# Performance work log

Hardware: AMD Instinct MI355X
Metric: run time of the kernel (lower is better)

## Reference

```python
import jax, jax.numpy as jnp
import numpy as np

HUGE = jnp.float32(1e31)   # ops.HUGE_INT
EPS = 1e-20
B, AN = 1024, 256
D = 256            # emb_dim
HD = 512           # history_dim
AD = 2 * D         # action_dim
NE, NR = 100000, 400


def setup_inputs() -> dict:
    key = jax.random.key(0)
    ks = jax.random.split(key, 12)
    e = jax.random.randint(ks[0], (B,), 0, NE)
    q = jax.random.randint(ks[1], (B,), 0, NR)
    hstate = jax.random.normal(ks[2], (B, HD), dtype=jnp.float32)
    r_space = jax.random.randint(ks[3], (B, AN), 0, NR)
    e_space = jax.random.randint(ks[4], (B, AN), 0, NE)
    # binary action mask; guarantee at least one valid action per row
    action_mask = (jax.random.uniform(ks[5], (B, AN)) > 0.2).astype(jnp.float32)
    action_mask = action_mask.at[:, 0].set(1.0)
    entity_emb = jax.random.normal(ks[6], (NE, D), dtype=jnp.float32) * 0.02
    relation_emb = jax.random.normal(ks[7], (NR, D), dtype=jnp.float32) * 0.02
    W1 = jax.random.normal(ks[8], (2 * D + HD, AD), dtype=jnp.float32) * (1.0 / np.sqrt(2 * D + HD))
    b1 = jnp.zeros((AD,), dtype=jnp.float32)
    W2 = jax.random.normal(ks[9], (AD, AD), dtype=jnp.float32) * (1.0 / np.sqrt(AD))
    b2 = jnp.zeros((AD,), dtype=jnp.float32)
    return {"e": e, "q": q, "hstate": hstate, "r_space": r_space,
            "e_space": e_space, "action_mask": action_mask,
            "entity_emb": entity_emb, "relation_emb": relation_emb,
            "W1": W1, "b1": b1, "W2": W2, "b2": b2}


def reference(e, q, hstate, r_space, e_space, action_mask,
              entity_emb, relation_emb, W1, b1, W2, b2):
    Q = relation_emb[q]                       # [B, D]
    E = entity_emb[e]                         # [B, D]
    X = jnp.concatenate([E, hstate, Q], axis=-1)          # [B, 2D+HD]
    X = jax.nn.relu(X @ W1 + b1)                          # [B, AD]
    X2 = X @ W2 + b2                                      # [B, AD]
    # action embeddings: [rel_emb[r]; ent_emb[e]] per padded action slot
    A = jnp.concatenate([relation_emb[r_space], entity_emb[e_space]], axis=-1)  # [B, AN, AD]
    scores = jnp.einsum('bad,bd->ba', A, X2) - (1.0 - action_mask) * HUGE      # [B, AN]
    action_dist = jax.nn.softmax(scores, axis=-1)
    entropy = -jnp.sum(action_dist * jnp.log(jnp.clip(action_dist, EPS)), axis=-1)  # [B]
    return action_dist, entropy
```

## Files before the change

kernel.cpp:

```cpp
#include <hip/hip_runtime.h>
#include <math.h>

#define NB   1024
#define NACT 256
#define DIM  256
#define HDIM 512
#define ADIM 512
#define KTOT 1024
#define KSPL 8

#define BM 64
#define BN 64
#define BK 32
#define LDA 68
#define LDB 68

__global__ __launch_bounds__(256) void gemm1_splitk(
    const int* __restrict__ e, const int* __restrict__ q,
    const float* __restrict__ hstate,
    const float* __restrict__ ent, const float* __restrict__ rel,
    const float* __restrict__ W1, float* __restrict__ Hpart)
{
    __shared__ float As[BK][LDA];
    __shared__ float Bs[BK][LDB];
    const int tid  = threadIdx.x;
    const int col0 = blockIdx.x * BN;
    const int row0 = blockIdx.y * BM;
    const int kc   = blockIdx.z;
    const int kbase = kc * (KTOT / KSPL);
    const int tx4  = (tid & 15) * 4;
    const int ty4  = (tid >> 4) * 4;
    float acc[4][4] = {};

    for (int k0 = 0; k0 < KTOT / KSPL; k0 += BK) {
        const int kglob = kbase + k0;
        #pragma unroll
        for (int s = 0; s < 2; ++s) {
            const int idx = tid * 2 + s;
            const int m   = idx >> 3;
            const int kf  = (idx & 7) * 4;
            const int b   = row0 + m;
            const int kk2 = kglob + kf;
            const float* src;
            if (kbase < DIM)             src = ent + (size_t)e[b] * DIM + kk2;
            else if (kbase < DIM + HDIM) src = hstate + (size_t)b * HDIM + (kk2 - DIM);
            else                         src = rel + (size_t)q[b] * DIM + (kk2 - DIM - HDIM);
            const float4 v = *(const float4*)src;
            As[kf + 0][m] = v.x;
            As[kf + 1][m] = v.y;
            As[kf + 2][m] = v.z;
            As[kf + 3][m] = v.w;
        }
        #pragma unroll
        for (int s = 0; s < 2; ++s) {
            const int idx = tid * 2 + s;
            const int k   = idx >> 4;
            const int n4  = (idx & 15) * 4;
            const float4 v = *(const float4*)(W1 + (size_t)(kglob + k) * ADIM + col0 + n4);
            *(float4*)(&Bs[k][n4]) = v;
        }
        __syncthreads();
        #pragma unroll
        for (int kk = 0; kk < BK; ++kk) {
            const float4 a4 = *(const float4*)(&As[kk][ty4]);
            const float4 b4 = *(const float4*)(&Bs[kk][tx4]);
            const float a[4] = {a4.x, a4.y, a4.z, a4.w};
            const float bb[4] = {b4.x, b4.y, b4.z, b4.w};
            #pragma unroll
            for (int i = 0; i < 4; ++i)
                #pragma unroll
                for (int j = 0; j < 4; ++j)
                    acc[i][j] += a[i] * bb[j];
        }
        __syncthreads();
    }
    float* dst = Hpart + (size_t)kc * NB * ADIM;
    #pragma unroll
    for (int i = 0; i < 4; ++i) {
        float4 o = {acc[i][0], acc[i][1], acc[i][2], acc[i][3]};
        *(float4*)(dst + (size_t)(row0 + ty4 + i) * ADIM + col0 + tx4) = o;
    }
}

__global__ __launch_bounds__(256) void gemm2_splitk(
    const float* __restrict__ Hpart, const float* __restrict__ b1,
    const float* __restrict__ W2, float* __restrict__ X2part)
{
    __shared__ float As[BK][LDA];
    __shared__ float Bs[BK][LDB];
    const int tid  = threadIdx.x;
    const int col0 = blockIdx.x * BN;
    const int row0 = blockIdx.y * BM;
    const int kc   = blockIdx.z;
    const int tx4  = (tid & 15) * 4;
    const int ty4  = (tid >> 4) * 4;
    float acc[4][4] = {};

    for (int k0 = 0; k0 < ADIM / KSPL; k0 += BK) {
        const int kglob = kc * (ADIM / KSPL) + k0;
        #pragma unroll
        for (int s = 0; s < 2; ++s) {
            const int idx = tid * 2 + s;
            const int m   = idx >> 3;
            const int kf  = (idx & 7) * 4;
            const int b   = row0 + m;
            const size_t off = (size_t)b * ADIM + kglob + kf;
            float4 v = *(const float4*)(b1 + kglob + kf);
            #pragma unroll
            for (int z = 0; z < KSPL; ++z) {
                const float4 p = *(const float4*)(Hpart + (size_t)z * NB * ADIM + off);
                v.x += p.x; v.y += p.y; v.z += p.z; v.w += p.w;
            }
            v.x = fmaxf(v.x, 0.0f);
            v.y = fmaxf(v.y, 0.0f);
            v.z = fmaxf(v.z, 0.0f);
            v.w = fmaxf(v.w, 0.0f);
            As[kf + 0][m] = v.x;
            As[kf + 1][m] = v.y;
            As[kf + 2][m] = v.z;
            As[kf + 3][m] = v.w;
        }
        #pragma unroll
        for (int s = 0; s < 2; ++s) {
            const int idx = tid * 2 + s;
            const int k   = idx >> 4;
            const int n4  = (idx & 15) * 4;
            const float4 v = *(const float4*)(W2 + (size_t)(kglob + k) * ADIM + col0 + n4);
            *(float4*)(&Bs[k][n4]) = v;
        }
        __syncthreads();
        #pragma unroll
        for (int kk = 0; kk < BK; ++kk) {
            const float4 a4 = *(const float4*)(&As[kk][ty4]);
            const float4 b4 = *(const float4*)(&Bs[kk][tx4]);
            const float a[4] = {a4.x, a4.y, a4.z, a4.w};
            const float bb[4] = {b4.x, b4.y, b4.z, b4.w};
            #pragma unroll
            for (int i = 0; i < 4; ++i)
                #pragma unroll
                for (int j = 0; j < 4; ++j)
                    acc[i][j] += a[i] * bb[j];
        }
        __syncthreads();
    }
    float* dst = X2part + (size_t)kc * NB * ADIM;
    #pragma unroll
    for (int i = 0; i < 4; ++i) {
        float4 o = {acc[i][0], acc[i][1], acc[i][2], acc[i][3]};
        *(float4*)(dst + (size_t)(row0 + ty4 + i) * ADIM + col0 + tx4) = o;
    }
}

__global__ __launch_bounds__(512) void scores_kernel(
    const int* __restrict__ r_space, const int* __restrict__ e_space,
    const float* __restrict__ amask,
    const float* __restrict__ ent, const float* __restrict__ rel,
    const float* __restrict__ X2part, const float* __restrict__ b2,
    float* __restrict__ dist_out, float* __restrict__ ent_out)
{
    const int b    = blockIdx.x;
    const int tid  = threadIdx.x;
    const int wave = tid >> 6;
    const int lane = tid & 63;

    __shared__ float xs[ADIM];
    __shared__ float sc[NACT];
    __shared__ float red1[8], red2[8], red3[8];

    if (tid < ADIM / 4) {
        float4 v = ((const float4*)b2)[tid];
        #pragma unroll
        for (int z = 0; z < KSPL; ++z) {
            const float4 p = ((const float4*)(X2part + (size_t)z * NB * ADIM + (size_t)b * ADIM))[tid];
            v.x += p.x; v.y += p.y; v.z += p.z; v.w += p.w;
        }
        ((float4*)xs)[tid] = v;
    }
    __syncthreads();

    const float4 xr = ((const float4*)xs)[lane];
    const float4 xe = ((const float4*)(xs + DIM))[lane];

    const int abase = wave * 32;
    for (int a0 = abase; a0 < abase + 32; a0 += 8) {
        float p[8];
        #pragma unroll
        for (int i = 0; i < 8; ++i) {
            const int r  = r_space[(size_t)b * NACT + a0 + i];
            const int ei = e_space[(size_t)b * NACT + a0 + i];
            const float4 rv = ((const float4*)(rel + (size_t)r  * DIM))[lane];
            const float4 ev = ((const float4*)(ent + (size_t)ei * DIM))[lane];
            p[i] = rv.x * xr.x + rv.y * xr.y + rv.z * xr.z + rv.w * xr.w
                 + ev.x * xe.x + ev.y * xe.y + ev.z * xe.z + ev.w * xe.w;
        }
        #pragma unroll
        for (int off = 32; off; off >>= 1) {
            #pragma unroll
            for (int i = 0; i < 8; ++i) p[i] += __shfl_xor(p[i], off);
        }
        if (lane < 8) sc[a0 + lane] = p[lane];
    }
    __syncthreads();

    float s = -3.0e38f;
    if (tid < NACT) {
        const float m = amask[(size_t)b * NACT + tid];
        s = sc[tid] - (1.0f - m) * 1e31f;
    }

    float mx = s;
    #pragma unroll
    for (int off = 32; off; off >>= 1) mx = fmaxf(mx, __shfl_xor(mx, off));
    if (lane == 0) red1[wave] = mx;
    __syncthreads();
    mx = red1[0];
    #pragma unroll
    for (int w = 1; w < 8; ++w) mx = fmaxf(mx, red1[w]);

    const float ex = (tid < NACT) ? expf(s - mx) : 0.0f;
    float sum = ex;
    #pragma unroll
    for (int off = 32; off; off >>= 1) sum += __shfl_xor(sum, off);
    if (lane == 0) red2[wave] = sum;
    __syncthreads();
    sum = ((red2[0] + red2[1]) + (red2[2] + red2[3]))
        + ((red2[4] + red2[5]) + (red2[6] + red2[7]));

    const float d = ex / sum;
    if (tid < NACT) dist_out[(size_t)b * NACT + tid] = d;

    float t = (tid < NACT) ? d * logf(fmaxf(d, 1e-20f)) : 0.0f;
    #pragma unroll
    for (int off = 32; off; off >>= 1) t += __shfl_xor(t, off);
    if (lane == 0) red3[wave] = t;
    __syncthreads();
    if (tid == 0)
        ent_out[b] = -(((red3[0] + red3[1]) + (red3[2] + red3[3]))
                     + ((red3[4] + red3[5]) + (red3[6] + red3[7])));
}

extern "C" void kernel_launch(void* const* d_in, const int* in_sizes, int n_in,
                              void* d_out, int out_size, void* d_ws, size_t ws_size,
                              hipStream_t stream) {
    const int*   e       = (const int*)d_in[0];
    const int*   q       = (const int*)d_in[1];
    const float* hstate  = (const float*)d_in[2];
    const int*   r_space = (const int*)d_in[3];
    const int*   e_space = (const int*)d_in[4];
    const float* amask   = (const float*)d_in[5];
    const float* ent     = (const float*)d_in[6];
    const float* rel     = (const float*)d_in[7];
    const float* W1      = (const float*)d_in[8];
    const float* b1      = (const float*)d_in[9];
    const float* W2      = (const float*)d_in[10];
    const float* b2      = (const float*)d_in[11];

    float* Hpart  = (float*)d_ws;
    float* X2part = Hpart + (size_t)KSPL * NB * ADIM;
    float* dist   = (float*)d_out;
    float* entr   = dist + (size_t)NB * NACT;

    gemm1_splitk<<<dim3(ADIM / BN, NB / BM, KSPL), 256, 0, stream>>>(e, q, hstate, ent, rel, W1, Hpart);
    gemm2_splitk<<<dim3(ADIM / BN, NB / BM, KSPL), 256, 0, stream>>>(Hpart, b1, W2, X2part);
    scores_kernel<<<NB, 512, 0, stream>>>(r_space, e_space, amask, ent, rel, X2part, b2, dist, entr);
}
```

Measured before the change: 241.1 us.

## Convert embedding tables to bf16 each call, pipeline GEMM loads, split out reduce

The first GEMM kernel now also converts the full entity and relation tables to bf16 on every call. The scores kernel then gathers half-width rows for its per-action dot products, which cuts gather bandwidth at the cost of a full-table read and write each call and some precision loss. Both GEMMs get register prefetch of the next K tile to overlap global loads with compute. The split-K reduction, bias and ReLU move into a separate kernel instead of being recomputed in every gemm2 block. Index arrays are staged in shared memory.

```diff
diff --git a/kernel.cpp b/kernel.cpp
--- a/kernel.cpp
+++ b/kernel.cpp
@@ -8,6 +8,8 @@
 #define ADIM 512
 #define KTOT 1024
 #define KSPL 8
+#define NE   100000
+#define NR   400
 
 #define BM 64
 #define BN 64
@@ -15,56 +17,179 @@
 #define LDA 68
 #define LDB 68
 
+__device__ __forceinline__ unsigned short f2bf(float f) {
+    unsigned int u = __float_as_uint(f);
+    u += 0x7FFF + ((u >> 16) & 1);
+    return (unsigned short)(u >> 16);
+}
+__device__ __forceinline__ float bf2f(unsigned short u) {
+    return __uint_as_float(((unsigned int)u) << 16);
+}
+
 __global__ __launch_bounds__(256) void gemm1_splitk(
     const int* __restrict__ e, const int* __restrict__ q,
     const float* __restrict__ hstate,
     const float* __restrict__ ent, const float* __restrict__ rel,
-    const float* __restrict__ W1, float* __restrict__ Hpart)
+    const float* __restrict__ W1, float* __restrict__ Hpart,
+    ushort* __restrict__ entbf, ushort* __restrict__ relbf)
+{
+    const int tid = threadIdx.x;
+    {
+        const int flat = blockIdx.x + blockIdx.y * gridDim.x
+                       + blockIdx.z * gridDim.x * gridDim.y;
+        const float4* src = (const float4*)ent;
+        ushort4* dst = (ushort4*)entbf;
+        const int start = flat * 6250;
+        #pragma unroll 4
+        for (int j = start + tid; j < start + 6250; j += 256) {
+            const float4 v = src[j];
+            ushort4 o;
+            o.x = f2bf(v.x); o.y = f2bf(v.y); o.z = f2bf(v.z); o.w = f2bf(v.w);
+            dst[j] = o;
+        }
+        if (tid < 25) {
+            const int j = flat * 25 + tid;
+            const float4 v = ((const float4*)rel)[j];
+            ushort4 o;
+            o.x = f2bf(v.x); o.y = f2bf(v.y); o.z = f2bf(v.z); o.w = f2bf(v.w);
+            ((ushort4*)relbf)[j] = o;
+        }
+    }
+
+    __shared__ float As[BK][LDA];
+    __shared__ float Bs[BK][LDB];
+    const int col0 = blockIdx.x * BN;
+    const int row0 = blockIdx.y * BM;
+    const int kbase = blockIdx.z * (KTOT / KSPL);
+    const int tx4 = (tid & 15) * 4;
+    const int ty4 = (tid >> 4) * 4;
+
+    const int am  = tid & 63;
+    const int kf0 = (tid >> 6) * 4;
+    const float* abase;
+    if (kbase < DIM)             abase = ent + (size_t)e[row0 + am] * DIM + kbase;
+    else if (kbase < DIM + HDIM) abase = hstate + (size_t)(row0 + am) * HDIM + (kbase - DIM);
+    else                         abase = rel + (size_t)q[row0 + am] * DIM + (kbase - DIM - HDIM);
+
+    const int kb0 = tid >> 4;
+    const float* bbase = W1 + col0 + tx4;
+
+    float4 pa0 = *(const float4*)(abase + kf0);
+    float4 pa1 = *(const float4*)(abase + kf0 + 16);
+    float4 pb0 = *(const float4*)(bbase + (size_t)(kbase + kb0) * ADIM);
+    float4 pb1 = *(const float4*)(bbase + (size_t)(kbase + kb0 + 16) * ADIM);
+
+    float acc[4][4] = {};
+    #pragma unroll
+    for (int it = 0; it < (KTOT / KSPL) / BK; ++it) {
+        As[kf0 + 0][am] = pa0.x;
+        As[kf0 + 1][am] = pa0.y;
+        As[kf0 + 2][am] = pa0.z;
+        As[kf0 + 3][am] = pa0.w;
+        As[kf0 + 16][am] = pa1.x;
+        As[kf0 + 17][am] = pa1.y;
+        As[kf0 + 18][am] = pa1.z;
+        As[kf0 + 19][am] = pa1.w;
+        *(float4*)(&Bs[kb0][tx4])      = pb0;
+        *(float4*)(&Bs[kb0 + 16][tx4]) = pb1;
+        __syncthreads();
+        if (it < (KTOT / KSPL) / BK - 1) {
+            const int ko = (it + 1) * BK;
+            pa0 = *(const float4*)(abase + ko + kf0);
+            pa1 = *(const float4*)(abase + ko + kf0 + 16);
+            pb0 = *(const float4*)(bbase + (size_t)(kbase + ko + kb0) * ADIM);
+            pb1 = *(const float4*)(bbase + (size_t)(kbase + ko + kb0 + 16) * ADIM);
+        }
+        #pragma unroll
+        for (int kk = 0; kk < BK; ++kk) {
+            const float4 a4 = *(const float4*)(&As[kk][ty4]);
+            const float4 b4 = *(const float4*)(&Bs[kk][tx4]);
+            const float a[4]  = {a4.x, a4.y, a4.z, a4.w};
+            const float bb[4] = {b4.x, b4.y, b4.z, b4.w};
+            #pragma unroll
+            for (int i = 0; i < 4; ++i)
+                #pragma unroll
+                for (int j = 0; j < 4; ++j)
+                    acc[i][j] += a[i] * bb[j];
+        }
+        __syncthreads();
+    }
+    float* dst = Hpart + (size_t)blockIdx.z * NB * ADIM;
+    #pragma unroll
+    for (int i = 0; i < 4; ++i) {
+        float4 o = {acc[i][0], acc[i][1], acc[i][2], acc[i][3]};
+        *(float4*)(dst + (size_t)(row0 + ty4 + i) * ADIM + col0 + tx4) = o;
+    }
+}
+
+__global__ __launch_bounds__(256) void reduce_relu(
+    const float* __restrict__ Hpart, const float* __restrict__ b1,
+    float* __restrict__ Hred)
+{
+    const int i = blockIdx.x * 256 + threadIdx.x;
+    float4 v = ((const float4*)b1)[i & 127];
+    #pragma unroll
+    for (int z = 0; z < KSPL; ++z) {
+        const float4 p = ((const float4*)Hpart)[(size_t)z * (NB * ADIM / 4) + i];
+        v.x += p.x; v.y += p.y; v.z += p.z; v.w += p.w;
+    }
+    v.x = fmaxf(v.x, 0.0f);
+    v.y = fmaxf(v.y, 0.0f);
+    v.z = fmaxf(v.z, 0.0f);
+    v.w = fmaxf(v.w, 0.0f);
+    ((float4*)Hred)[i] = v;
+}
+
+__global__ __launch_bounds__(256) void gemm2_splitk(
+    const float* __restrict__ Hred, const float* __restrict__ W2,
+    float* __restrict__ X2part)
 {
     __shared__ float As[BK][LDA];
     __shared__ float Bs[BK][LDB];
     const int tid  = threadIdx.x;
     const int col0 = blockIdx.x * BN;
     const int row0 = blockIdx.y * BM;
-    const int kc   = blockIdx.z;
-    const int kbase = kc * (KTOT / KSPL);
-    const int tx4  = (tid & 15) * 4;
-    const int ty4  = (tid >> 4) * 4;
+    const int kbase = blockIdx.z * (ADIM / KSPL);
+    const int tx4 = (tid & 15) * 4;
+    const int ty4 = (tid >> 4) * 4;
+
+    const int am  = tid & 63;
+    const int kf0 = (tid >> 6) * 4;
+    const float* abase = Hred + (size_t)(row0 + am) * ADIM + kbase;
+    const int kb0 = tid >> 4;
+    const float* bbase = W2 + col0 + tx4;
+
+    float4 pa0 = *(const float4*)(abase + kf0);
+    float4 pa1 = *(const float4*)(abase + kf0 + 16);
+    float4 pb0 = *(const float4*)(bbase + (size_t)(kbase + kb0) * ADIM);
+    float4 pb1 = *(const float4*)(bbase + (size_t)(kbase + kb0 + 16) * ADIM);
+
     float acc[4][4] = {};
-
-    for (int k0 = 0; k0 < KTOT / KSPL; k0 += BK) {
-        const int kglob = kbase + k0;
-        #pragma unroll
-        for (int s = 0; s < 2; ++s) {
-            const int idx = tid * 2 + s;
-            const int m   = idx >> 3;
-            const int kf  = (idx & 7) * 4;
-            const int b   = row0 + m;
-            const int kk2 = kglob + kf;
-            const float* src;
-            if (kbase < DIM)             src = ent + (size_t)e[b] * DIM + kk2;
-            else if (kbase < DIM + HDIM) src = hstate + (size_t)b * HDIM + (kk2 - DIM);
-            else                         src = rel + (size_t)q[b] * DIM + (kk2 - DIM - HDIM);
-            const float4 v = *(const float4*)src;
-            As[kf + 0][m] = v.x;
-            As[kf + 1][m] = v.y;
-            As[kf + 2][m] = v.z;
-            As[kf + 3][m] = v.w;
-        }
-        #pragma unroll
-        for (int s = 0; s < 2; ++s) {
-            const int idx = tid * 2 + s;
-            const int k   = idx >> 4;
-            const int n4  = (idx & 15) * 4;
-            const float4 v = *(const float4*)(W1 + (size_t)(kglob + k) * ADIM + col0 + n4);
-            *(float4*)(&Bs[k][n4]) = v;
-        }
+    #pragma unroll
+    for (int it = 0; it < (ADIM / KSPL) / BK; ++it) {
+        As[kf0 + 0][am] = pa0.x;
+        As[kf0 + 1][am] = pa0.y;
+        As[kf0 + 2][am] = pa0.z;
+        As[kf0 + 3][am] = pa0.w;
+        As[kf0 + 16][am] = pa1.x;
+        As[kf0 + 17][am] = pa1.y;
+        As[kf0 + 18][am] = pa1.z;
+        As[kf0 + 19][am] = pa1.w;
+        *(float4*)(&Bs[kb0][tx4])      = pb0;
+        *(float4*)(&Bs[kb0 + 16][tx4]) = pb1;
         __syncthreads();
+        if (it < (ADIM / KSPL) / BK - 1) {
+            const int ko = (it + 1) * BK;
+            pa0 = *(const float4*)(abase + ko + kf0);
+            pa1 = *(const float4*)(abase + ko + kf0 + 16);
+            pb0 = *(const float4*)(bbase + (size_t)(kbase + ko + kb0) * ADIM);
+            pb1 = *(const float4*)(bbase + (size_t)(kbase + ko + kb0 + 16) * ADIM);
+        }
         #pragma unroll
         for (int kk = 0; kk < BK; ++kk) {
             const float4 a4 = *(const float4*)(&As[kk][ty4]);
             const float4 b4 = *(const float4*)(&Bs[kk][tx4]);
-            const float a[4] = {a4.x, a4.y, a4.z, a4.w};
+            const float a[4]  = {a4.x, a4.y, a4.z, a4.w};
             const float bb[4] = {b4.x, b4.y, b4.z, b4.w};
             #pragma unroll
             for (int i = 0; i < 4; ++i)
@@ -74,7 +199,7 @@
         }
         __syncthreads();
     }
-    float* dst = Hpart + (size_t)kc * NB * ADIM;
+    float* dst = X2part + (size_t)blockIdx.z * NB * ADIM;
     #pragma unroll
     for (int i = 0; i < 4; ++i) {
         float4 o = {acc[i][0], acc[i][1], acc[i][2], acc[i][3]};
@@ -82,79 +207,10 @@
     }
 }
 
-__global__ __launch_bounds__(256) void gemm2_splitk(
-    const float* __restrict__ Hpart, const float* __restrict__ b1,
-    const float* __restrict__ W2, float* __restrict__ X2part)
-{
-    __shared__ float As[BK][LDA];
-    __shared__ float Bs[BK][LDB];
-    const int tid  = threadIdx.x;
-    const int col0 = blockIdx.x * BN;
-    const int row0 = blockIdx.y * BM;
-    const int kc   = blockIdx.z;
-    const int tx4  = (tid & 15) * 4;
-    const int ty4  = (tid >> 4) * 4;
-    float acc[4][4] = {};
-
-    for (int k0 = 0; k0 < ADIM / KSPL; k0 += BK) {
-        const int kglob = kc * (ADIM / KSPL) + k0;
-        #pragma unroll
-        for (int s = 0; s < 2; ++s) {
-            const int idx = tid * 2 + s;
-            const int m   = idx >> 3;
-            const int kf  = (idx & 7) * 4;
-            const int b   = row0 + m;
-            const size_t off = (size_t)b * ADIM + kglob + kf;
-            float4 v = *(const float4*)(b1 + kglob + kf);
-            #pragma unroll
-            for (int z = 0; z < KSPL; ++z) {
-                const float4 p = *(const float4*)(Hpart + (size_t)z * NB * ADIM + off);
-                v.x += p.x; v.y += p.y; v.z += p.z; v.w += p.w;
-            }
-            v.x = fmaxf(v.x, 0.0f);
-            v.y = fmaxf(v.y, 0.0f);
-            v.z = fmaxf(v.z, 0.0f);
-            v.w = fmaxf(v.w, 0.0f);
-            As[kf + 0][m] = v.x;
-            As[kf + 1][m] = v.y;
-            As[kf + 2][m] = v.z;
-            As[kf + 3][m] = v.w;
-        }
-        #pragma unroll
-        for (int s = 0; s < 2; ++s) {
-            const int idx = tid * 2 + s;
-            const int k   = idx >> 4;
-            const int n4  = (idx & 15) * 4;
-            const float4 v = *(const float4*)(W2 + (size_t)(kglob + k) * ADIM + col0 + n4);
-            *(float4*)(&Bs[k][n4]) = v;
-        }
-        __syncthreads();
-        #pragma unroll
-        for (int kk = 0; kk < BK; ++kk) {
-            const float4 a4 = *(const float4*)(&As[kk][ty4]);
-            const float4 b4 = *(const float4*)(&Bs[kk][tx4]);
-            const float a[4] = {a4.x, a4.y, a4.z, a4.w};
-            const float bb[4] = {b4.x, b4.y, b4.z, b4.w};
-            #pragma unroll
-            for (int i = 0; i < 4; ++i)
-                #pragma unroll
-                for (int j = 0; j < 4; ++j)
-                    acc[i][j] += a[i] * bb[j];
-        }
-        __syncthreads();
-    }
-    float* dst = X2part + (size_t)kc * NB * ADIM;
-    #pragma unroll
-    for (int i = 0; i < 4; ++i) {
-        float4 o = {acc[i][0], acc[i][1], acc[i][2], acc[i][3]};
-        *(float4*)(dst + (size_t)(row0 + ty4 + i) * ADIM + col0 + tx4) = o;
-    }
-}
-
 __global__ __launch_bounds__(512) void scores_kernel(
     const int* __restrict__ r_space, const int* __restrict__ e_space,
     const float* __restrict__ amask,
-    const float* __restrict__ ent, const float* __restrict__ rel,
+    const ushort* __restrict__ relbf, const ushort* __restrict__ entbf,
     const float* __restrict__ X2part, const float* __restrict__ b2,
     float* __restrict__ dist_out, float* __restrict__ ent_out)
 {
@@ -165,13 +221,17 @@
 
     __shared__ float xs[ADIM];
     __shared__ float sc[NACT];
+    __shared__ int   ridx[NACT];
+    __shared__ int   eidx[NACT];
     __shared__ float red1[8], red2[8], red3[8];
 
+    if (tid < NACT)       ridx[tid] = r_space[(size_t)b * NACT + tid];
+    else                  eidx[tid - NACT] = e_space[(size_t)b * NACT + tid - NACT];
     if (tid < ADIM / 4) {
         float4 v = ((const float4*)b2)[tid];
         #pragma unroll
         for (int z = 0; z < KSPL; ++z) {
-            const float4 p = ((const float4*)(X2part + (size_t)z * NB * ADIM + (size_t)b * ADIM))[tid];
+            const float4 p = ((const float4*)X2part)[(size_t)z * (NB * ADIM / 4) + b * (ADIM / 4) + tid];
             v.x += p.x; v.y += p.y; v.z += p.z; v.w += p.w;
         }
         ((float4*)xs)[tid] = v;
@@ -183,22 +243,29 @@
 
     const int abase = wave * 32;
     for (int a0 = abase; a0 < abase + 32; a0 += 8) {
+        ushort4 rv[8], ev[8];
+        #pragma unroll
+        for (int i = 0; i < 8; ++i) {
+            rv[i] = ((const ushort4*)relbf)[(size_t)ridx[a0 + i] * (DIM / 4) + lane];
+            ev[i] = ((const ushort4*)entbf)[(size_t)eidx[a0 + i] * (DIM / 4) + lane];
+        }
         float p[8];
         #pragma unroll
         for (int i = 0; i < 8; ++i) {
-            const int r  = r_space[(size_t)b * NACT + a0 + i];
-            const int ei = e_space[(size_t)b * NACT + a0 + i];
-            const float4 rv = ((const float4*)(rel + (size_t)r  * DIM))[lane];
-            const float4 ev = ((const float4*)(ent + (size_t)ei * DIM))[lane];
-            p[i] = rv.x * xr.x + rv.y * xr.y + rv.z * xr.z + rv.w * xr.w
-                 + ev.x * xe.x + ev.y * xe.y + ev.z * xe.z + ev.w * xe.w;
+            p[i] = bf2f(rv[i].x) * xr.x + bf2f(rv[i].y) * xr.y
+                 + bf2f(rv[i].z) * xr.z + bf2f(rv[i].w) * xr.w
+                 + bf2f(ev[i].x) * xe.x + bf2f(ev[i].y) * xe.y
+                 + bf2f(ev[i].z) * xe.z + bf2f(ev[i].w) * xe.w;
         }
         #pragma unroll
         for (int off = 32; off; off >>= 1) {
             #pragma unroll
             for (int i = 0; i < 8; ++i) p[i] += __shfl_xor(p[i], off);
         }
-        if (lane < 8) sc[a0 + lane] = p[lane];
+        float out = p[0];
+        #pragma unroll
+        for (int i = 1; i < 8; ++i) out = (lane == i) ? p[i] : out;
+        if (lane < 8) sc[a0 + lane] = out;
     }
     __syncthreads();
 
@@ -257,10 +324,16 @@
 
     float* Hpart  = (float*)d_ws;
     float* X2part = Hpart + (size_t)KSPL * NB * ADIM;
+    float* Hred   = X2part + (size_t)KSPL * NB * ADIM;
+    ushort* entbf = (ushort*)(Hred + (size_t)NB * ADIM);
+    ushort* relbf = entbf + (size_t)NE * DIM;
     float* dist   = (float*)d_out;
     float* entr   = dist + (size_t)NB * NACT;
 
-    gemm1_splitk<<<dim3(ADIM / BN, NB / BM, KSPL), 256, 0, stream>>>(e, q, hstate, ent, rel, W1, Hpart);
-    gemm2_splitk<<<dim3(ADIM / BN, NB / BM, KSPL), 256, 0, stream>>>(Hpart, b1, W2, X2part);
-    scores_kernel<<<NB, 512, 0, stream>>>(r_space, e_space, amask, ent, rel, X2part, b2, dist, entr);
-}
+    gemm1_splitk<<<dim3(ADIM / BN, NB / BM, KSPL), 256, 0, stream>>>(
+        e, q, hstate, ent, rel, W1, Hpart, entbf, relbf);
+    reduce_relu<<<dim3(NB * ADIM / 4 / 256), 256, 0, stream>>>(Hpart, b1, Hred);
+    gemm2_splitk<<<dim3(ADIM / BN, NB / BM, KSPL), 256, 0, stream>>>(Hred, W2, X2part);
+    scores_kernel<<<NB, 512, 0, stream>>>(
+        r_space, e_space, amask, relbf, entbf, X2part, b2, dist, entr);
+}
```

After: 237.7 us. About the same (-1.4%).

## Convert to bf16, use MFMA GEMMs, and gather bf16 embeddings for scores

Applied to the files above, without the earlier changes.

Adds prep kernels that convert the entity and relation tables, the concatenated MLP input, and transposed W1/W2 to bf16 on every call. The fp32 split-K GEMMs and their partial-sum buffers are replaced by a single-pass bf16 MFMA GEMM with fused bias/ReLU. The scores kernel now gathers bf16 embedding rows with indices staged in shared memory, halving gather bytes. In exchange, the full entity table (about 100 MB) is converted on every call, and reduced precision may affect softmax accuracy.

```diff
diff --git a/kernel.cpp b/kernel.cpp
--- a/kernel.cpp
+++ b/kernel.cpp
@@ -7,155 +7,147 @@
 #define HDIM 512
 #define ADIM 512
 #define KTOT 1024
-#define KSPL 8
-
-#define BM 64
-#define BN 64
-#define BK 32
-#define LDA 68
-#define LDB 68
-
-__global__ __launch_bounds__(256) void gemm1_splitk(
+#define NE   100000
+#define NR   400
+
+typedef __attribute__((ext_vector_type(8))) short bf16x8;
+typedef __attribute__((ext_vector_type(4))) float f32x4;
+
+__device__ __forceinline__ unsigned short f2bf(float f) {
+    unsigned int u = __float_as_uint(f);
+    u += 0x7FFF + ((u >> 16) & 1);
+    return (unsigned short)(u >> 16);
+}
+__device__ __forceinline__ float bf2f(unsigned short u) {
+    return __uint_as_float(((unsigned int)u) << 16);
+}
+
+__global__ __launch_bounds__(256) void prep_stream(
+    const float* __restrict__ ent, const float* __restrict__ rel,
+    const float* __restrict__ hstate,
     const int* __restrict__ e, const int* __restrict__ q,
-    const float* __restrict__ hstate,
-    const float* __restrict__ ent, const float* __restrict__ rel,
-    const float* __restrict__ W1, float* __restrict__ Hpart)
-{
-    __shared__ float As[BK][LDA];
-    __shared__ float Bs[BK][LDB];
+    ushort* __restrict__ entbf, ushort* __restrict__ relbf,
+    ushort* __restrict__ Xbf)
+{
+    const int blk = blockIdx.x, tid = threadIdx.x;
+    if (blk < 1024) {
+        const float4* src = (const float4*)ent;
+        ushort4* dst = (ushort4*)entbf;
+        const int start = blk * 6250;
+        for (int j = start + tid; j < start + 6250; j += 256) {
+            const float4 v = src[j];
+            ushort4 o = {f2bf(v.x), f2bf(v.y), f2bf(v.z), f2bf(v.w)};
+            dst[j] = o;
+        }
+    } else if (blk < 1028) {
+        const float4* src = (const float4*)rel;
+        ushort4* dst = (ushort4*)relbf;
+        const int start = (blk - 1024) * 6400;
+        for (int j = start + tid; j < start + 6400; j += 256) {
+            const float4 v = src[j];
+            ushort4 o = {f2bf(v.x), f2bf(v.y), f2bf(v.z), f2bf(v.w)};
+            dst[j] = o;
+        }
+    } else {
+        const int b0 = (blk - 1028) * 16;
+        const int c = tid * 4;
+        for (int r = 0; r < 16; ++r) {
+            const int b = b0 + r;
+            float4 v;
+            if (c < DIM)             v = *(const float4*)(ent + (size_t)e[b] * DIM + c);
+            else if (c < DIM + HDIM) v = *(const float4*)(hstate + (size_t)b * HDIM + (c - DIM));
+            else                     v = *(const float4*)(rel + (size_t)q[b] * DIM + (c - DIM - HDIM));
+            ushort4 o = {f2bf(v.x), f2bf(v.y), f2bf(v.z), f2bf(v.w)};
+            *(ushort4*)(Xbf + (size_t)b * KTOT + c) = o;
+        }
+    }
+}
+
+__global__ __launch_bounds__(256) void prep_transpose(
+    const float* __restrict__ W1, const float* __restrict__ W2,
+    ushort* __restrict__ W1T, ushort* __restrict__ W2T)
+{
+    __shared__ float t[64][68];
+    const int z = blockIdx.z;
+    if (z && blockIdx.x >= 8) return;
+    const int Kd = z ? 512 : 1024;
+    const float* in = z ? W2 : W1;
+    ushort* out = z ? W2T : W1T;
+    const int k0 = blockIdx.x * 64, n0 = blockIdx.y * 64;
+    const int tid = threadIdx.x;
+    const int kr = tid >> 2, c = tid & 3;
+    #pragma unroll
+    for (int j = 0; j < 4; ++j) {
+        const float4 v = *(const float4*)(in + (size_t)(k0 + kr) * ADIM + n0 + c * 16 + j * 4);
+        *(float4*)&t[kr][c * 16 + j * 4] = v;
+    }
+    __syncthreads();
+    const int nr = tid >> 2;
+    ushort tmp[16];
+    #pragma unroll
+    for (int kk = 0; kk < 16; ++kk) tmp[kk] = f2bf(t[c * 16 + kk][nr]);
+    *(uint4*)(out + (size_t)(n0 + nr) * Kd + k0 + c * 16)     = *(uint4*)&tmp[0];
+    *(uint4*)(out + (size_t)(n0 + nr) * Kd + k0 + c * 16 + 8) = *(uint4*)&tmp[8];
+}
+
+template<int K, bool RELU_BF16>
+__global__ __launch_bounds__(256) void gemm_mfma(
+    const ushort* __restrict__ A, const ushort* __restrict__ Bt,
+    const float* __restrict__ bias, ushort* __restrict__ Cbf,
+    float* __restrict__ Cf, int ldc)
+{
+    __shared__ __align__(16) ushort Als[64][40];
+    __shared__ __align__(16) ushort Bls[64][40];
     const int tid  = threadIdx.x;
-    const int col0 = blockIdx.x * BN;
-    const int row0 = blockIdx.y * BM;
-    const int kc   = blockIdx.z;
-    const int kbase = kc * (KTOT / KSPL);
-    const int tx4  = (tid & 15) * 4;
-    const int ty4  = (tid >> 4) * 4;
-    float acc[4][4] = {};
-
-    for (int k0 = 0; k0 < KTOT / KSPL; k0 += BK) {
-        const int kglob = kbase + k0;
-        #pragma unroll
-        for (int s = 0; s < 2; ++s) {
-            const int idx = tid * 2 + s;
-            const int m   = idx >> 3;
-            const int kf  = (idx & 7) * 4;
-            const int b   = row0 + m;
-            const int kk2 = kglob + kf;
-            const float* src;
-            if (kbase < DIM)             src = ent + (size_t)e[b] * DIM + kk2;
-            else if (kbase < DIM + HDIM) src = hstate + (size_t)b * HDIM + (kk2 - DIM);
-            else                         src = rel + (size_t)q[b] * DIM + (kk2 - DIM - HDIM);
-            const float4 v = *(const float4*)src;
-            As[kf + 0][m] = v.x;
-            As[kf + 1][m] = v.y;
-            As[kf + 2][m] = v.z;
-            As[kf + 3][m] = v.w;
-        }
-        #pragma unroll
-        for (int s = 0; s < 2; ++s) {
-            const int idx = tid * 2 + s;
-            const int k   = idx >> 4;
-            const int n4  = (idx & 15) * 4;
-            const float4 v = *(const float4*)(W1 + (size_t)(kglob + k) * ADIM + col0 + n4);
-            *(float4*)(&Bs[k][n4]) = v;
-        }
+    const int n0   = blockIdx.x * 64;
+    const int m0   = blockIdx.y * 64;
+    const int wave = tid >> 6, lane = tid & 63;
+    const int q    = lane >> 4, l15 = lane & 15;
+    const int sm   = tid >> 2, sc = tid & 3;
+
+    const uint4* ga = (const uint4*)(A  + (size_t)(m0 + sm) * K) + sc;
+    const uint4* gb = (const uint4*)(Bt + (size_t)(n0 + sm) * K) + sc;
+
+    f32x4 acc[4];
+    #pragma unroll
+    for (int mt = 0; mt < 4; ++mt) acc[mt] = (f32x4){0.f, 0.f, 0.f, 0.f};
+
+    uint4 pa = ga[0], pb = gb[0];
+    for (int it = 0; it < K / 32; ++it) {
+        *(uint4*)&Als[sm][sc * 8] = pa;
+        *(uint4*)&Bls[sm][sc * 8] = pb;
         __syncthreads();
-        #pragma unroll
-        for (int kk = 0; kk < BK; ++kk) {
-            const float4 a4 = *(const float4*)(&As[kk][ty4]);
-            const float4 b4 = *(const float4*)(&Bs[kk][tx4]);
-            const float a[4] = {a4.x, a4.y, a4.z, a4.w};
-            const float bb[4] = {b4.x, b4.y, b4.z, b4.w};
-            #pragma unroll
-            for (int i = 0; i < 4; ++i)
-                #pragma unroll
-                for (int j = 0; j < 4; ++j)
-                    acc[i][j] += a[i] * bb[j];
+        if (it + 1 < K / 32) {
+            pa = ga[(it + 1) * 4];
+            pb = gb[(it + 1) * 4];
+        }
+        const bf16x8 bfrag = *(const bf16x8*)&Bls[wave * 16 + l15][q * 8];
+        #pragma unroll
+        for (int mt = 0; mt < 4; ++mt) {
+            const bf16x8 afrag = *(const bf16x8*)&Als[mt * 16 + l15][q * 8];
+            acc[mt] = __builtin_amdgcn_mfma_f32_16x16x32_bf16(afrag, bfrag, acc[mt], 0, 0, 0);
         }
         __syncthreads();
     }
-    float* dst = Hpart + (size_t)kc * NB * ADIM;
-    #pragma unroll
-    for (int i = 0; i < 4; ++i) {
-        float4 o = {acc[i][0], acc[i][1], acc[i][2], acc[i][3]};
-        *(float4*)(dst + (size_t)(row0 + ty4 + i) * ADIM + col0 + tx4) = o;
-    }
-}
-
-__global__ __launch_bounds__(256) void gemm2_splitk(
-    const float* __restrict__ Hpart, const float* __restrict__ b1,
-    const float* __restrict__ W2, float* __restrict__ X2part)
-{
-    __shared__ float As[BK][LDA];
-    __shared__ float Bs[BK][LDB];
-    const int tid  = threadIdx.x;
-    const int col0 = blockIdx.x * BN;
-    const int row0 = blockIdx.y * BM;
-    const int kc   = blockIdx.z;
-    const int tx4  = (tid & 15) * 4;
-    const int ty4  = (tid >> 4) * 4;
-    float acc[4][4] = {};
-
-    for (int k0 = 0; k0 < ADIM / KSPL; k0 += BK) {
-        const int kglob = kc * (ADIM / KSPL) + k0;
-        #pragma unroll
-        for (int s = 0; s < 2; ++s) {
-            const int idx = tid * 2 + s;
-            const int m   = idx >> 3;
-            const int kf  = (idx & 7) * 4;
-            const int b   = row0 + m;
-            const size_t off = (size_t)b * ADIM + kglob + kf;
-            float4 v = *(const float4*)(b1 + kglob + kf);
-            #pragma unroll
-            for (int z = 0; z < KSPL; ++z) {
-                const float4 p = *(const float4*)(Hpart + (size_t)z * NB * ADIM + off);
-                v.x += p.x; v.y += p.y; v.z += p.z; v.w += p.w;
-            }
-            v.x = fmaxf(v.x, 0.0f);
-            v.y = fmaxf(v.y, 0.0f);
-            v.z = fmaxf(v.z, 0.0f);
-            v.w = fmaxf(v.w, 0.0f);
-            As[kf + 0][m] = v.x;
-            As[kf + 1][m] = v.y;
-            As[kf + 2][m] = v.z;
-            As[kf + 3][m] = v.w;
-        }
-        #pragma unroll
-        for (int s = 0; s < 2; ++s) {
-            const int idx = tid * 2 + s;
-            const int k   = idx >> 4;
-            const int n4  = (idx & 15) * 4;
-            const float4 v = *(const float4*)(W2 + (size_t)(kglob + k) * ADIM + col0 + n4);
-            *(float4*)(&Bs[k][n4]) = v;
-        }
-        __syncthreads();
-        #pragma unroll
-        for (int kk = 0; kk < BK; ++kk) {
-            const float4 a4 = *(const float4*)(&As[kk][ty4]);
-            const float4 b4 = *(const float4*)(&Bs[kk][tx4]);
-            const float a[4] = {a4.x, a4.y, a4.z, a4.w};
-            const float bb[4] = {b4.x, b4.y, b4.z, b4.w};
-            #pragma unroll
-            for (int i = 0; i < 4; ++i)
-                #pragma unroll
-                for (int j = 0; j < 4; ++j)
-                    acc[i][j] += a[i] * bb[j];
-        }
-        __syncthreads();
-    }
-    float* dst = X2part + (size_t)kc * NB * ADIM;
-    #pragma unroll
-    for (int i = 0; i < 4; ++i) {
-        float4 o = {acc[i][0], acc[i][1], acc[i][2], acc[i][3]};
-        *(float4*)(dst + (size_t)(row0 + ty4 + i) * ADIM + col0 + tx4) = o;
+    const int n = n0 + wave * 16 + l15;
+    const float bv = bias[n];
+    #pragma unroll
+    for (int mt = 0; mt < 4; ++mt) {
+        #pragma unroll
+        for (int r = 0; r < 4; ++r) {
+            const int m = m0 + mt * 16 + q * 4 + r;
+            const float v = acc[mt][r] + bv;
+            if (RELU_BF16) Cbf[(size_t)m * ldc + n] = f2bf(fmaxf(v, 0.0f));
+            else           Cf [(size_t)m * ldc + n] = v;
+        }
     }
 }
 
 __global__ __launch_bounds__(512) void scores_kernel(
     const int* __restrict__ r_space, const int* __restrict__ e_space,
     const float* __restrict__ amask,
-    const float* __restrict__ ent, const float* __restrict__ rel,
-    const float* __restrict__ X2part, const float* __restrict__ b2,
+    const ushort* __restrict__ relbf, const ushort* __restrict__ entbf,
+    const float* __restrict__ X2,
     float* __restrict__ dist_out, float* __restrict__ ent_out)
 {
     const int b    = blockIdx.x;
@@ -165,17 +157,14 @@
 
     __shared__ float xs[ADIM];
     __shared__ float sc[NACT];
+    __shared__ int   ridx[NACT];
+    __shared__ int   eidx[NACT];
     __shared__ float red1[8], red2[8], red3[8];
 
-    if (tid < ADIM / 4) {
-        float4 v = ((const float4*)b2)[tid];
-        #pragma unroll
-        for (int z = 0; z < KSPL; ++z) {
-            const float4 p = ((const float4*)(X2part + (size_t)z * NB * ADIM + (size_t)b * ADIM))[tid];
-            v.x += p.x; v.y += p.y; v.z += p.z; v.w += p.w;
-        }
-        ((float4*)xs)[tid] = v;
-    }
+    if (tid < NACT) ridx[tid] = r_space[(size_t)b * NACT + tid];
+    else            eidx[tid - NACT] = e_space[(size_t)b * NACT + tid - NACT];
+    if (tid < ADIM / 4)
+        ((float4*)xs)[tid] = ((const float4*)(X2 + (size_t)b * ADIM))[tid];
     __syncthreads();
 
     const float4 xr = ((const float4*)xs)[lane];
@@ -183,22 +172,29 @@
 
     const int abase = wave * 32;
     for (int a0 = abase; a0 < abase + 32; a0 += 8) {
+        ushort4 rv[8], ev[8];
+        #pragma unroll
+        for (int i = 0; i < 8; ++i) {
+            rv[i] = ((const ushort4*)relbf)[(size_t)ridx[a0 + i] * (DIM / 4) + lane];
+            ev[i] = ((const ushort4*)entbf)[(size_t)eidx[a0 + i] * (DIM / 4) + lane];
+        }
         float p[8];
         #pragma unroll
         for (int i = 0; i < 8; ++i) {
-            const int r  = r_space[(size_t)b * NACT + a0 + i];
-            const int ei = e_space[(size_t)b * NACT + a0 + i];
-            const float4 rv = ((const float4*)(rel + (size_t)r  * DIM))[lane];
-            const float4 ev = ((const float4*)(ent + (size_t)ei * DIM))[lane];
-            p[i] = rv.x * xr.x + rv.y * xr.y + rv.z * xr.z + rv.w * xr.w
-                 + ev.x * xe.x + ev.y * xe.y + ev.z * xe.z + ev.w * xe.w;
+            p[i] = bf2f(rv[i].x) * xr.x + bf2f(rv[i].y) * xr.y
+                 + bf2f(rv[i].z) * xr.z + bf2f(rv[i].w) * xr.w
+                 + bf2f(ev[i].x) * xe.x + bf2f(ev[i].y) * xe.y
+                 + bf2f(ev[i].z) * xe.z + bf2f(ev[i].w) * xe.w;
         }
         #pragma unroll
         for (int off = 32; off; off >>= 1) {
             #pragma unroll
             for (int i = 0; i < 8; ++i) p[i] += __shfl_xor(p[i], off);
         }
-        if (lane < 8) sc[a0 + lane] = p[lane];
+        float out = p[0];
+        #pragma unroll
+        for (int i = 1; i < 8; ++i) out = (lane == i) ? p[i] : out;
+        if (lane < 8) sc[a0 + lane] = out;
     }
     __syncthreads();
 
@@ -255,12 +251,22 @@
     const float* W2      = (const float*)d_in[10];
     const float* b2      = (const float*)d_in[11];
 
-    float* Hpart  = (float*)d_ws;
-    float* X2part = Hpart + (size_t)KSPL * NB * ADIM;
-    float* dist   = (float*)d_out;
-    float* entr   = dist + (size_t)NB * NACT;
-
-    gemm1_splitk<<<dim3(ADIM / BN, NB / BM, KSPL), 256, 0, stream>>>(e, q, hstate, ent, rel, W1, Hpart);
-    gemm2_splitk<<<dim3(ADIM / BN, NB / BM, KSPL), 256, 0, stream>>>(Hpart, b1, W2, X2part);
-    scores_kernel<<<NB, 512, 0, stream>>>(r_space, e_space, amask, ent, rel, X2part, b2, dist, entr);
-}
+    ushort* Xbf   = (ushort*)d_ws;
+    ushort* W1T   = Xbf   + (size_t)NB * KTOT;
+    ushort* W2T   = W1T   + (size_t)ADIM * KTOT;
+    ushort* Hbf   = W2T   + (size_t)ADIM * ADIM;
+    ushort* entbf = Hbf   + (size_t)NB * ADIM;
+    ushort* relbf = entbf + (size_t)NE * DIM;
+    float*  X2    = (float*)(relbf + (size_t)NR * DIM);
+    float*  dist  = (float*)d_out;
+    float*  entr  = dist + (size_t)NB * NACT;
+
+    prep_stream<<<1092, 256, 0, stream>>>(ent, rel, hstate, e, q, entbf, relbf, Xbf);
+    prep_transpose<<<dim3(16, 8, 2), 256, 0, stream>>>(W1, W2, W1T, W2T);
+    gemm_mfma<KTOT, true><<<dim3(ADIM / 64, NB / 64), 256, 0, stream>>>(
+        Xbf, W1T, b1, Hbf, nullptr, ADIM);
+    gemm_mfma<ADIM, false><<<dim3(ADIM / 64, NB / 64), 256, 0, stream>>>(
+        Hbf, W2T, b2, nullptr, X2, ADIM);
+    scores_kernel<<<NB, 512, 0, stream>>>(
+        r_space, e_space, amask, relbf, entbf, X2, dist, entr);
+}
```

Measured after the change: 234.7 us. 2.6% less time.
